# Kernel optimization log

Measured on AMD Instinct MI355X. Metric: run time of the kernel, lower is better.

Reference implementation:

```python
import jax, jax.numpy as jnp
import numpy as np

N_NODES = 100_000
N_EDGES = 1_600_000
VOCAB = 10_000
NUM_GRAPHS = 512
D_EMB, D_HID, D_OUT = 64, 128, 64


def _sage_conv(h, src, dst, Wl, b, Wr, num_nodes):
    """PyG SAGEConv with mean aggregation: lin_l(mean_{j in N(i)} x_j) + lin_r(x_i)."""
    msgs = h[src]                                               # [E, D]
    agg = jax.ops.segment_sum(msgs, dst, num_segments=num_nodes)
    deg = jax.ops.segment_sum(jnp.ones((src.shape[0], 1), h.dtype), dst,
                              num_segments=num_nodes)
    agg = agg / jnp.maximum(deg, 1.0)                           # mean over neighbors
    return agg @ Wl + b + h @ Wr


def setup_inputs() -> dict:
    key = jax.random.key(0)
    ks = jax.random.split(key, 12)
    x = jax.random.randint(ks[0], (N_NODES,), 0, VOCAB)
    edge_index = jax.random.randint(ks[1], (2, N_EDGES), 0, N_NODES)
    batch = jnp.sort(jax.random.randint(ks[2], (N_NODES,), 0, NUM_GRAPHS))
    edge_attr = jax.random.uniform(ks[3], (N_EDGES, 1), dtype=jnp.float32)
    embed = jax.random.normal(ks[4], (VOCAB, D_EMB), dtype=jnp.float32) * 0.02
    W1l = jax.random.normal(ks[5], (D_EMB, D_HID), dtype=jnp.float32) / np.sqrt(D_EMB)
    b1 = jnp.zeros((D_HID,), jnp.float32)
    W1r = jax.random.normal(ks[6], (D_EMB, D_HID), dtype=jnp.float32) / np.sqrt(D_EMB)
    W2l = jax.random.normal(ks[7], (D_HID, D_OUT), dtype=jnp.float32) / np.sqrt(D_HID)
    b2 = jnp.zeros((D_OUT,), jnp.float32)
    W2r = jax.random.normal(ks[8], (D_HID, D_OUT), dtype=jnp.float32) / np.sqrt(D_HID)
    return {"x": x, "edge_index": edge_index, "batch": batch, "edge_attr": edge_attr,
            "embed": embed, "W1l": W1l, "b1": b1, "W1r": W1r,
            "W2l": W2l, "b2": b2, "W2r": W2r}


def reference(x, edge_index, batch, edge_attr, embed, W1l, b1, W1r, W2l, b2, W2r):
    # edge_attr is passed in the original forward but PyG SAGEConv ignores edge weights.
    src, dst = edge_index[0], edge_index[1]
    h = embed[x]                                                # [N, 64]
    h = jax.nn.relu(_sage_conv(h, src, dst, W1l, b1, W1r, N_NODES))  # [N, 128]
    h = _sage_conv(h, src, dst, W2l, b2, W2r, N_NODES)          # [N, 64]
    out = jax.ops.segment_max(h, batch, num_segments=NUM_GRAPHS)  # [G, 64]
    return out
```

## Files before the change

kernel.cpp:

```cpp
#include <hip/hip_runtime.h>
#include <cstdint>

#define NN 100000
#define NE 1600000
#define NG 512
#define NP 100032
#define VOCAB 10000
#define NBUK 256
#define BSZ 391
#define CAP 7680
#define EPB 1563

typedef unsigned short u16;
typedef u16      u16x4  __attribute__((ext_vector_type(4)));
typedef u16      u16x8  __attribute__((ext_vector_type(8)));
typedef __bf16   bf16x8 __attribute__((ext_vector_type(8)));
typedef float    f32x4  __attribute__((ext_vector_type(4)));
typedef float    f32x2  __attribute__((ext_vector_type(2)));

__device__ __forceinline__ u16 f2bf(float f) {
    unsigned u = __float_as_uint(f);
    unsigned r = ((u >> 16) & 1u) + 0x7FFFu;
    return (u16)((u + r) >> 16);
}
__device__ __forceinline__ float bf2f(u16 h) {
    return __uint_as_float(((unsigned)h) << 16);
}

__device__ __forceinline__ unsigned encF(float f) {
    unsigned s = __float_as_uint(f);
    return (s & 0x80000000u) ? ~s : (s | 0x80000000u);
}
__device__ __forceinline__ float decF(unsigned m) {
    unsigned s = (m & 0x80000000u) ? (m ^ 0x80000000u) : ~m;
    return __uint_as_float(s);
}

template <bool HI>
__device__ __forceinline__ void gather8(const int* __restrict__ csr, int beg, int end,
                                        const u16* __restrict__ table, int lane,
                                        f32x2 acc[4]) {
    if (beg >= end) return;
    const int sub = lane >> 3, g8 = (lane & 7) * 8;
    auto ld = [&](int b0) -> bf16x8 {
        bf16x8 v = {};
        int idx = b0 + sub;
        if (idx < end) {
            int e = csr[idx];
            int r = HI ? (e >> 17) : (e & 0x1FFFF);
            v = *(const bf16x8*)(table + (size_t)r * 64 + g8);
        }
        return v;
    };
    auto acc8 = [&](const bf16x8& v) {
        #pragma unroll
        for (int k = 0; k < 4; ++k) {
            f32x2 w = {(float)v[2 * k], (float)v[2 * k + 1]};
            acc[k] += w;
        }
    };
    bf16x8 c0 = ld(beg);
    bf16x8 c1 = ld(beg + 8);
    for (int b0 = beg + 16; b0 < end; b0 += 8) {
        bf16x8 n = ld(b0);
        acc8(c0);
        c0 = c1;
        c1 = n;
    }
    acc8(c0);
    acc8(c1);
}

__device__ __forceinline__ float reduce_dim(const f32x2 acc[4], float* sT, int lane) {
    const int sub = lane >> 3, g8 = (lane & 7) * 8;
    #pragma unroll
    for (int k = 0; k < 4; ++k)
        *(f32x2*)&sT[sub * 66 + g8 + 2 * k] = acc[k];
    float t = 0.0f;
    #pragma unroll
    for (int sg = 0; sg < 8; ++sg) t += sT[sg * 66 + lane];
    return t;
}

__device__ __forceinline__ void prepW_body(const float* __restrict__ Wa,
                                           const float* __restrict__ Wb,
                                           int mode, u16* __restrict__ Wpk, int idx) {
    int fid = idx >> 6, lane = idx & 63;
    int cT = fid >> 2, ks = fid & 3;
    int quad = lane >> 4, l16 = lane & 15;
    int n = cT * 16 + l16;
    u16x8 v;
    #pragma unroll
    for (int j = 0; j < 8; ++j) {
        int k = ks * 32 + quad * 8 + j;
        float f = (mode == 0) ? (k < 64 ? Wa[k * 128 + n] : Wb[(k - 64) * 128 + n])
                              : (n < 64 ? Wa[k * 64 + n] : Wb[k * 64 + (n - 64)]);
        v[j] = f2bf(f);
    }
    *(u16x8*)(Wpk + idx * 8) = v;
}

__global__ __launch_bounds__(256) void k_fused(
        const int* __restrict__ ei, int* __restrict__ gcur,
        unsigned* __restrict__ gbuf,
        const float* __restrict__ emb, u16* __restrict__ embB,
        const float* __restrict__ W1l, const float* __restrict__ W1r,
        u16* __restrict__ Wpk1,
        const float* __restrict__ W2l, const float* __restrict__ W2r,
        u16* __restrict__ Wpk2, unsigned* __restrict__ om) {
    const int bid = blockIdx.x, t = threadIdx.x;
    if (bid >= 1024) {
        if (bid < 1649) {
            int i = (bid - 1024) * 1024 + t * 4;
            float4 f = *(const float4*)(emb + i);
            u16x4 o = {f2bf(f.x), f2bf(f.y), f2bf(f.z), f2bf(f.w)};
            *(u16x4*)(embB + i) = o;
        } else if (bid < 1657) {
            prepW_body(W1l, W1r, 0, Wpk1, (bid - 1649) * 256 + t);
        } else if (bid < 1665) {
            prepW_body(W2l, W2r, 1, Wpk2, (bid - 1657) * 256 + t);
        } else {
            om[(bid - 1665) * 256 + t] = 0x007FFFFFu;
        }
        return;
    }
    __shared__ int cnt[NBUK];
    __shared__ int start[NBUK];
    __shared__ int gbase[NBUK];
    __shared__ int wsum[4];
    __shared__ unsigned buf[EPB];
    __shared__ unsigned char bkt[EPB];
    const int e0 = bid * EPB;
    const int tc = min(NE - e0, EPB);
    cnt[t] = 0;
    __syncthreads();
    unsigned ent[7];
    unsigned char eb[7];
    u16 rk[7];
    int nm = 0;
    for (int i = t; i < tc; i += 256) {
        int dst = ei[NE + e0 + i];
        int src = ei[e0 + i];
        unsigned b = (unsigned)dst / BSZ;
        unsigned dl = (unsigned)dst - b * BSZ;
        ent[nm] = (dl << 17) | (unsigned)src;
        eb[nm] = (unsigned char)b;
        rk[nm] = (u16)atomicAdd(&cnt[b], 1);
        ++nm;
    }
    __syncthreads();
    {
        int c = cnt[t];
        int s = c;
        #pragma unroll
        for (int d = 1; d < 64; d <<= 1) {
            int v = __shfl_up(s, d, 64);
            if ((t & 63) >= d) s += v;
        }
        if ((t & 63) == 63) wsum[t >> 6] = s;
        __syncthreads();
        int pre = 0;
        #pragma unroll
        for (int w = 0; w < 4; ++w) pre += (w < (t >> 6)) ? wsum[w] : 0;
        start[t] = pre + s - c;
        gbase[t] = atomicAdd(&gcur[t], c);
    }
    __syncthreads();
    for (int k = 0; k < nm; ++k) {
        int pos = start[eb[k]] + rk[k];
        buf[pos] = ent[k];
        bkt[pos] = eb[k];
    }
    __syncthreads();
    for (int i = t; i < tc; i += 256) {
        unsigned b = bkt[i];
        gbuf[(size_t)b * CAP + gbase[b] + (i - start[b])] = buf[i];
    }
}

__global__ __launch_bounds__(512) void k_csr(const unsigned* __restrict__ gbuf,
                                             const int* __restrict__ gcur,
                                             const int* __restrict__ x,
                                             int* __restrict__ off,
                                             int* __restrict__ csr) {
    __shared__ int hist[BSZ];
    __shared__ int curL[BSZ];
    __shared__ int wsum[8];
    __shared__ int sred[8];
    const int b = blockIdx.x, t = threadIdx.x;
    if (t < BSZ) hist[t] = 0;
    __syncthreads();
    const int size = gcur[b];
    const unsigned* gb = gbuf + (size_t)b * CAP;
    for (int i = t; i < size; i += 512)
        atomicAdd(&hist[gb[i] >> 17], 1);
    {
        int v = (t < 256 && t < b) ? gcur[t] : 0;
        #pragma unroll
        for (int d = 32; d > 0; d >>= 1) v += __shfl_down(v, d, 64);
        if ((t & 63) == 0) sred[t >> 6] = v;
    }
    __syncthreads();
    const int gbase = sred[0] + sred[1] + sred[2] + sred[3];
    int h = (t < BSZ) ? hist[t] : 0;
    int s = h;
    #pragma unroll
    for (int d = 1; d < 64; d <<= 1) {
        int v = __shfl_up(s, d, 64);
        if ((t & 63) >= d) s += v;
    }
    if ((t & 63) == 63) wsum[t >> 6] = s;
    __syncthreads();
    int pre = 0;
    #pragma unroll
    for (int w = 0; w < 7; ++w) pre += (w < (t >> 6)) ? wsum[w] : 0;
    if (t < BSZ) {
        int ex = gbase + pre + s - h;
        curL[t] = ex;
        int g0 = b * BSZ;
        if (g0 + t <= NN) off[g0 + t] = ex;
    }
    __syncthreads();
    for (int i = t; i < size; i += 512) {
        unsigned ent = gb[i];
        int src = (int)(ent & 0x1FFFFu);
        int dl  = (int)(ent >> 17);
        int pos = atomicAdd(&curL[dl], 1);
        csr[pos] = src | (x[src] << 17);
    }
}

__global__ __launch_bounds__(256, 8) void k_gg(
        const int* __restrict__ off, const int* __restrict__ csr,
        const int* __restrict__ x, const u16* __restrict__ embB,
        const u16* __restrict__ Wpk1, const u16* __restrict__ Wpk2,
        const float* __restrict__ b1,
        u16* __restrict__ P, u16* __restrict__ Q) {
    __shared__ __align__(16) u16 sA1[32][136];
    __shared__ __align__(16) u16 sH1[32][136];
    const int wv = threadIdx.x >> 6, lane = threadIdx.x & 63;
    const int quad = lane >> 4, l16 = lane & 15;
    float* sT = (float*)&sH1[0][0] + wv * 528;
    const int base = blockIdx.x * 32;
    for (int it = 0; it < 8; ++it) {
        int lr = wv * 8 + it;
        int node = base + lr;
        if (node < NN) {
            int beg = off[node], end = off[node + 1];
            f32x2 acc[4] = {{0.f, 0.f}, {0.f, 0.f}, {0.f, 0.f}, {0.f, 0.f}};
            gather8<true>(csr, beg, end, embB, lane, acc);
            float tv = reduce_dim(acc, sT, lane);
            sA1[lr][lane] = f2bf(tv / fmaxf((float)(end - beg), 1.0f));
            sA1[lr][64 + lane] = embB[x[node] * 64 + lane];
        } else {
            sA1[lr][lane] = 0;
            sA1[lr][64 + lane] = 0;
        }
    }
    __syncthreads();
    u16x8 bf1[2][4];
    #pragma unroll
    for (int ct = 0; ct < 2; ++ct)
        #pragma unroll
        for (int ks = 0; ks < 4; ++ks)
            bf1[ct][ks] = *(const u16x8*)(Wpk1 + (((wv * 2 + ct) * 4 + ks) * 64 + lane) * 8);
    f32x4 st1[2][2];
    #pragma unroll
    for (int rt = 0; rt < 2; ++rt) {
        u16x8 a[4];
        #pragma unroll
        for (int ks = 0; ks < 4; ++ks)
            a[ks] = *(const u16x8*)(&sA1[rt * 16 + l16][ks * 32 + quad * 8]);
        #pragma unroll
        for (int ct = 0; ct < 2; ++ct) {
            f32x4 acc = {0.f, 0.f, 0.f, 0.f};
            #pragma unroll
            for (int ks = 0; ks < 4; ++ks)
                acc = __builtin_amdgcn_mfma_f32_16x16x32_bf16(
                    __builtin_bit_cast(bf16x8, a[ks]),
                    __builtin_bit_cast(bf16x8, bf1[ct][ks]), acc, 0, 0, 0);
            st1[rt][ct] = acc;
        }
    }
    __syncthreads();
    #pragma unroll
    for (int rt = 0; rt < 2; ++rt)
        #pragma unroll
        for (int ct = 0; ct < 2; ++ct) {
            int col = wv * 32 + ct * 16 + l16;
            float bias = b1[col];
            int lr = rt * 16 + quad * 4;
            #pragma unroll
            for (int reg = 0; reg < 4; ++reg)
                sH1[lr + reg][col] = f2bf(fmaxf(st1[rt][ct][reg] + bias, 0.f));
        }
    __syncthreads();
    u16x8 bf2[2][4];
    #pragma unroll
    for (int ct = 0; ct < 2; ++ct)
        #pragma unroll
        for (int ks = 0; ks < 4; ++ks)
            bf2[ct][ks] = *(const u16x8*)(Wpk2 + (((wv * 2 + ct) * 4 + ks) * 64 + lane) * 8);
    #pragma unroll
    for (int rt = 0; rt < 2; ++rt) {
        u16x8 a[4];
        #pragma unroll
        for (int ks = 0; ks < 4; ++ks)
            a[ks] = *(const u16x8*)(&sH1[rt * 16 + l16][ks * 32 + quad * 8]);
        #pragma unroll
        for (int ct = 0; ct < 2; ++ct) {
            f32x4 acc = {0.f, 0.f, 0.f, 0.f};
            #pragma unroll
            for (int ks = 0; ks < 4; ++ks)
                acc = __builtin_amdgcn_mfma_f32_16x16x32_bf16(
                    __builtin_bit_cast(bf16x8, a[ks]),
                    __builtin_bit_cast(bf16x8, bf2[ct][ks]), acc, 0, 0, 0);
            int col = wv * 32 + ct * 16 + l16;
            int gr = base + rt * 16 + quad * 4;
            u16* dstT = (col < 64) ? P : Q;
            int c = col & 63;
            #pragma unroll
            for (int reg = 0; reg < 4; ++reg)
                dstT[(gr + reg) * 64 + c] = f2bf(acc[reg]);
        }
    }
}

__global__ __launch_bounds__(256, 8) void k_final(const int* __restrict__ off,
                                                  const int* __restrict__ csr,
                                                  const u16* __restrict__ P,
                                                  const u16* __restrict__ Q,
                                                  const float* __restrict__ b2,
                                                  const int* __restrict__ batch,
                                                  unsigned* __restrict__ om) {
    __shared__ float sTT[4][528];
    __shared__ float sR[4][64];
    __shared__ int sG[4];
    int wv = threadIdx.x >> 6, lane = threadIdx.x & 63;
    for (int grp = blockIdx.x; grp * 4 < NN; grp += gridDim.x) {
        int node = grp * 4 + wv;
        int beg = off[node], end = off[node + 1];
        f32x2 acc[4] = {{0.f, 0.f}, {0.f, 0.f}, {0.f, 0.f}, {0.f, 0.f}};
        gather8<false>(csr, beg, end, P, lane, acc);
        float t = reduce_dim(acc, sTT[wv], lane);
        float r = t / fmaxf((float)(end - beg), 1.0f) + b2[lane]
                + bf2f(Q[node * 64 + lane]);
        int g = batch[node];
        sR[wv][lane] = r;
        if (lane == 0) sG[wv] = g;
        __syncthreads();
        bool leader = (wv == 0) || (sG[wv - 1] != g);
        if (leader) {
            float m = r;
            for (int u = wv + 1; u < 4 && sG[u] == g; ++u) m = fmaxf(m, sR[u][lane]);
            atomicMax(&om[g * 64 + lane], encF(m));
        }
        __syncthreads();
    }
}

__global__ void k_decode(const unsigned* __restrict__ om, float* __restrict__ out) {
    int i = blockIdx.x * blockDim.x + threadIdx.x;
    if (i < NG * 64) out[i] = decF(om[i]);
}

extern "C" void kernel_launch(void* const* d_in, const int* in_sizes, int n_in,
                              void* d_out, int out_size, void* d_ws, size_t ws_size,
                              hipStream_t stream) {
    const int*   x     = (const int*)d_in[0];
    const int*   ei    = (const int*)d_in[1];
    const int*   batch = (const int*)d_in[2];
    const float* emb   = (const float*)d_in[4];
    const float* W1l   = (const float*)d_in[5];
    const float* b1    = (const float*)d_in[6];
    const float* W1r   = (const float*)d_in[7];
    const float* W2l   = (const float*)d_in[8];
    const float* b2    = (const float*)d_in[9];
    const float* W2r   = (const float*)d_in[10];
    float* out = (float*)d_out;

    char* p = (char*)d_ws;
    u16* P    = (u16*)p;               p += (size_t)NP * 64 * 2;
    u16* Q    = (u16*)p;               p += (size_t)NP * 64 * 2;
    int* csr  = (int*)p;               p += (size_t)NE * 4;
    unsigned* gbuf = (unsigned*)p;     p += (size_t)NBUK * CAP * 4;
    int* gcur = (int*)p;               p += NBUK * 4;
    int* off  = (int*)p;               p += (size_t)(NN + 1) * 4;
    u16* Wpk1 = (u16*)p;               p += 16384 * 2;
    u16* Wpk2 = (u16*)p;               p += 16384 * 2;
    u16* embB = (u16*)p;               p += (size_t)VOCAB * 64 * 2;
    unsigned* om = (unsigned*)p;

    hipMemsetAsync(gcur, 0, sizeof(int) * NBUK, stream);
    k_fused<<<1793, 256, 0, stream>>>(ei, gcur, gbuf, emb, embB,
                                      W1l, W1r, Wpk1, W2l, W2r, Wpk2, om);
    k_csr<<<NBUK, 512, 0, stream>>>(gbuf, gcur, x, off, csr);
    k_gg<<<NP / 32, 256, 0, stream>>>(off, csr, x, embB, Wpk1, Wpk2, b1, P, Q);
    k_final<<<2048, 256, 0, stream>>>(off, csr, P, Q, b2, batch, om);
    k_decode<<<(NG * 64 + 255) / 256, 256, 0, stream>>>(om, out);
}
```

Before: 213.8 us.

## Aggregate layer-2 messages per destination bucket in shared memory from unsorted buffer

Doubles the bucket count (512 buckets of 196 nodes) so each block's per-bucket aggregation buffer fits in LDS. The final layer now reads the unsorted bucket buffer directly and scatter-adds P rows into a shared-memory accumulator with LDS float atomics, instead of gathering through the CSR per node. The per-graph max is then computed with a running max per wave over contiguous nodes. This trades the sorted-CSR gather for LDS atomic contention, and uses only 512 blocks, which may limit parallelism.

```diff
diff --git a/kernel.cpp b/kernel.cpp
--- a/kernel.cpp
+++ b/kernel.cpp
@@ -6,10 +6,11 @@
 #define NG 512
 #define NP 100032
 #define VOCAB 10000
-#define NBUK 256
-#define BSZ 391
-#define CAP 7680
+#define NBUK 512
+#define BSZ 196
+#define CAP 4096
 #define EPB 1563
+#define SAG 66
 
 typedef unsigned short u16;
 typedef u16      u16x4  __attribute__((ext_vector_type(4)));
@@ -34,6 +35,14 @@
 __device__ __forceinline__ float decF(unsigned m) {
     unsigned s = (m & 0x80000000u) ? (m ^ 0x80000000u) : ~m;
     return __uint_as_float(s);
+}
+
+__device__ __forceinline__ void acc8(f32x2 acc[4], const bf16x8& v) {
+    #pragma unroll
+    for (int k = 0; k < 4; ++k) {
+        f32x2 w = {(float)v[2 * k], (float)v[2 * k + 1]};
+        acc[k] += w;
+    }
 }
 
 template <bool HI>
@@ -52,23 +61,16 @@
         }
         return v;
     };
-    auto acc8 = [&](const bf16x8& v) {
-        #pragma unroll
-        for (int k = 0; k < 4; ++k) {
-            f32x2 w = {(float)v[2 * k], (float)v[2 * k + 1]};
-            acc[k] += w;
-        }
-    };
     bf16x8 c0 = ld(beg);
     bf16x8 c1 = ld(beg + 8);
     for (int b0 = beg + 16; b0 < end; b0 += 8) {
         bf16x8 n = ld(b0);
-        acc8(c0);
+        acc8(acc, c0);
         c0 = c1;
         c1 = n;
     }
-    acc8(c0);
-    acc8(c1);
+    acc8(acc, c0);
+    acc8(acc, c1);
 }
 
 __device__ __forceinline__ float reduce_dim(const f32x2 acc[4], float* sT, int lane) {
@@ -128,14 +130,16 @@
     __shared__ int start[NBUK];
     __shared__ int gbase[NBUK];
     __shared__ int wsum[4];
+    __shared__ int wsum2[4];
     __shared__ unsigned buf[EPB];
-    __shared__ unsigned char bkt[EPB];
+    __shared__ u16 bkt[EPB];
     const int e0 = bid * EPB;
     const int tc = min(NE - e0, EPB);
     cnt[t] = 0;
+    cnt[t + 256] = 0;
     __syncthreads();
     unsigned ent[7];
-    unsigned char eb[7];
+    u16 eb[7];
     u16 rk[7];
     int nm = 0;
     for (int i = t; i < tc; i += 256) {
@@ -144,26 +148,33 @@
         unsigned b = (unsigned)dst / BSZ;
         unsigned dl = (unsigned)dst - b * BSZ;
         ent[nm] = (dl << 17) | (unsigned)src;
-        eb[nm] = (unsigned char)b;
+        eb[nm] = (u16)b;
         rk[nm] = (u16)atomicAdd(&cnt[b], 1);
         ++nm;
     }
     __syncthreads();
     {
-        int c = cnt[t];
-        int s = c;
+        int c0 = cnt[t], c1 = cnt[t + 256];
+        int s0 = c0, s1 = c1;
         #pragma unroll
         for (int d = 1; d < 64; d <<= 1) {
-            int v = __shfl_up(s, d, 64);
-            if ((t & 63) >= d) s += v;
-        }
-        if ((t & 63) == 63) wsum[t >> 6] = s;
+            int v0 = __shfl_up(s0, d, 64);
+            int v1 = __shfl_up(s1, d, 64);
+            if ((t & 63) >= d) { s0 += v0; s1 += v1; }
+        }
+        if ((t & 63) == 63) { wsum[t >> 6] = s0; wsum2[t >> 6] = s1; }
         __syncthreads();
-        int pre = 0;
-        #pragma unroll
-        for (int w = 0; w < 4; ++w) pre += (w < (t >> 6)) ? wsum[w] : 0;
-        start[t] = pre + s - c;
-        gbase[t] = atomicAdd(&gcur[t], c);
+        int pre0 = 0, pre1 = 0, T0 = 0;
+        #pragma unroll
+        for (int w = 0; w < 4; ++w) {
+            T0 += wsum[w];
+            pre0 += (w < (t >> 6)) ? wsum[w] : 0;
+            pre1 += (w < (t >> 6)) ? wsum2[w] : 0;
+        }
+        start[t] = pre0 + s0 - c0;
+        start[t + 256] = T0 + pre1 + s1 - c1;
+        gbase[t] = atomicAdd(&gcur[t], c0);
+        gbase[t + 256] = atomicAdd(&gcur[t + 256], c1);
     }
     __syncthreads();
     for (int k = 0; k < nm; ++k) {
@@ -178,24 +189,24 @@
     }
 }
 
-__global__ __launch_bounds__(512) void k_csr(const unsigned* __restrict__ gbuf,
+__global__ __launch_bounds__(256) void k_csr(const unsigned* __restrict__ gbuf,
                                              const int* __restrict__ gcur,
                                              const int* __restrict__ x,
                                              int* __restrict__ off,
                                              int* __restrict__ csr) {
     __shared__ int hist[BSZ];
     __shared__ int curL[BSZ];
-    __shared__ int wsum[8];
-    __shared__ int sred[8];
+    __shared__ int wsum[4];
+    __shared__ int sred[4];
     const int b = blockIdx.x, t = threadIdx.x;
     if (t < BSZ) hist[t] = 0;
     __syncthreads();
     const int size = gcur[b];
     const unsigned* gb = gbuf + (size_t)b * CAP;
-    for (int i = t; i < size; i += 512)
+    for (int i = t; i < size; i += 256)
         atomicAdd(&hist[gb[i] >> 17], 1);
     {
-        int v = (t < 256 && t < b) ? gcur[t] : 0;
+        int v = ((t < b) ? gcur[t] : 0) + ((t + 256 < b) ? gcur[t + 256] : 0);
         #pragma unroll
         for (int d = 32; d > 0; d >>= 1) v += __shfl_down(v, d, 64);
         if ((t & 63) == 0) sred[t >> 6] = v;
@@ -213,7 +224,7 @@
     __syncthreads();
     int pre = 0;
     #pragma unroll
-    for (int w = 0; w < 7; ++w) pre += (w < (t >> 6)) ? wsum[w] : 0;
+    for (int w = 0; w < 3; ++w) pre += (w < (t >> 6)) ? wsum[w] : 0;
     if (t < BSZ) {
         int ex = gbase + pre + s - h;
         curL[t] = ex;
@@ -221,7 +232,7 @@
         if (g0 + t <= NN) off[g0 + t] = ex;
     }
     __syncthreads();
-    for (int i = t; i < size; i += 512) {
+    for (int i = t; i < size; i += 256) {
         unsigned ent = gb[i];
         int src = (int)(ent & 0x1FFFFu);
         int dl  = (int)(ent >> 17);
@@ -326,37 +337,65 @@
     }
 }
 
-__global__ __launch_bounds__(256, 8) void k_final(const int* __restrict__ off,
-                                                  const int* __restrict__ csr,
-                                                  const u16* __restrict__ P,
-                                                  const u16* __restrict__ Q,
-                                                  const float* __restrict__ b2,
-                                                  const int* __restrict__ batch,
-                                                  unsigned* __restrict__ om) {
-    __shared__ float sTT[4][528];
-    __shared__ float sR[4][64];
-    __shared__ int sG[4];
-    int wv = threadIdx.x >> 6, lane = threadIdx.x & 63;
-    for (int grp = blockIdx.x; grp * 4 < NN; grp += gridDim.x) {
-        int node = grp * 4 + wv;
+__global__ __launch_bounds__(512, 4) void k_final2(
+        const unsigned* __restrict__ gbuf, const int* __restrict__ gcur,
+        const int* __restrict__ off, const u16* __restrict__ P,
+        const u16* __restrict__ Q, const float* __restrict__ b2,
+        const int* __restrict__ batch, unsigned* __restrict__ om) {
+    __shared__ float agg[BSZ * SAG];
+    const int b = blockIdx.x, t = threadIdx.x;
+    for (int i = t; i < BSZ * SAG; i += 512) agg[i] = 0.f;
+    __syncthreads();
+    const int size = gcur[b];
+    const unsigned* gb = gbuf + (size_t)b * CAP;
+    const int sub = t >> 3;
+    const int g8 = (t & 7) * 8;
+    for (int i = sub; i < size; i += 512) {
+        unsigned ent[8];
+        bf16x8 v[8];
+        #pragma unroll
+        for (int u = 0; u < 8; ++u) {
+            int idx = i + u * 64;
+            ent[u] = (idx < size) ? gb[idx] : 0xFFFFFFFFu;
+        }
+        #pragma unroll
+        for (int u = 0; u < 8; ++u) {
+            v[u] = bf16x8{};
+            if (ent[u] != 0xFFFFFFFFu)
+                v[u] = *(const bf16x8*)(P + (size_t)(ent[u] & 0x1FFFFu) * 64 + g8);
+        }
+        #pragma unroll
+        for (int u = 0; u < 8; ++u) {
+            if (ent[u] != 0xFFFFFFFFu) {
+                float* arow = &agg[(ent[u] >> 17) * SAG + g8];
+                #pragma unroll
+                for (int k = 0; k < 8; ++k)
+                    atomicAdd(&arow[k], (float)v[u][k]);
+            }
+        }
+    }
+    __syncthreads();
+    int wv = t >> 6, lane = t & 63;
+    float bias = b2[lane];
+    int n0 = wv * 25, n1 = min(n0 + 25, BSZ);
+    int gcur_ = -1;
+    float m = 0.0f;
+    for (int dl = n0; dl < n1; ++dl) {
+        int node = b * BSZ + dl;
+        if (node >= NN) break;
         int beg = off[node], end = off[node + 1];
-        f32x2 acc[4] = {{0.f, 0.f}, {0.f, 0.f}, {0.f, 0.f}, {0.f, 0.f}};
-        gather8<false>(csr, beg, end, P, lane, acc);
-        float t = reduce_dim(acc, sTT[wv], lane);
-        float r = t / fmaxf((float)(end - beg), 1.0f) + b2[lane]
-                + bf2f(Q[node * 64 + lane]);
+        float r = agg[dl * SAG + lane] / fmaxf((float)(end - beg), 1.0f)
+                + bias + bf2f(Q[node * 64 + lane]);
         int g = batch[node];
-        sR[wv][lane] = r;
-        if (lane == 0) sG[wv] = g;
-        __syncthreads();
-        bool leader = (wv == 0) || (sG[wv - 1] != g);
-        if (leader) {
-            float m = r;
-            for (int u = wv + 1; u < 4 && sG[u] == g; ++u) m = fmaxf(m, sR[u][lane]);
-            atomicMax(&om[g * 64 + lane], encF(m));
-        }
-        __syncthreads();
-    }
+        if (g != gcur_) {
+            if (gcur_ >= 0) atomicMax(&om[gcur_ * 64 + lane], encF(m));
+            gcur_ = g;
+            m = r;
+        } else {
+            m = fmaxf(m, r);
+        }
+    }
+    if (gcur_ >= 0) atomicMax(&om[gcur_ * 64 + lane], encF(m));
 }
 
 __global__ void k_decode(const unsigned* __restrict__ om, float* __restrict__ out) {
@@ -394,8 +433,8 @@
     hipMemsetAsync(gcur, 0, sizeof(int) * NBUK, stream);
     k_fused<<<1793, 256, 0, stream>>>(ei, gcur, gbuf, emb, embB,
                                       W1l, W1r, Wpk1, W2l, W2r, Wpk2, om);
-    k_csr<<<NBUK, 512, 0, stream>>>(gbuf, gcur, x, off, csr);
+    k_csr<<<NBUK, 256, 0, stream>>>(gbuf, gcur, x, off, csr);
     k_gg<<<NP / 32, 256, 0, stream>>>(off, csr, x, embB, Wpk1, Wpk2, b1, P, Q);
-    k_final<<<2048, 256, 0, stream>>>(off, csr, P, Q, b2, batch, om);
+    k_final2<<<NBUK, 512, 0, stream>>>(gbuf, gcur, off, P, Q, b2, batch, om);
     k_decode<<<(NG * 64 + 255) / 256, 256, 0, stream>>>(om, out);
 }
```

New measurement: 715.6 us. 235% more time.
